# Performance work log

Measured on AMD Instinct MI355X. Metric: run time of the kernel, lower is better.

The kernel has to match this reference:

```python
import jax, jax.numpy as jnp
import numpy as np

N_BINS = 15


def setup_inputs() -> dict:
    key = jax.random.key(0)
    k1, k2 = jax.random.split(key)
    probs = jax.random.uniform(k1, (1, 2, 4096, 4096), dtype=jnp.float32)
    labels = jax.random.randint(k2, (1, 1, 4096, 4096), 0, 2, dtype=jnp.int32)
    return {"probs": probs, "labels": labels}


def _bin_stats(conf, acc, boundaries):
    # bin i holds conf in (boundaries[i], boundaries[i+1]] -> searchsorted left - 1
    idx = jnp.searchsorted(boundaries, conf, side="left") - 1
    valid = (idx >= 0) & (idx < N_BINS)
    idx = jnp.where(valid, idx, N_BINS)  # route invalid (conf==0) to overflow bin
    vmask = valid.astype(conf.dtype)
    count = jax.ops.segment_sum(vmask, idx, num_segments=N_BINS + 1)[:N_BINS]
    csum = jax.ops.segment_sum(conf * vmask, idx, num_segments=N_BINS + 1)[:N_BINS]
    asum = jax.ops.segment_sum(acc * vmask, idx, num_segments=N_BINS + 1)[:N_BINS]
    return count, csum, asum


def reference(probs, labels):
    h, w = probs.shape[2], probs.shape[3]
    boundaries = jnp.linspace(0.0, 1.0, N_BINS + 1)
    conf0 = probs[0, 0].reshape(h * w)
    conf1 = probs[0, 1].reshape(h * w)
    lab = labels[0, 0].reshape(h * w)
    acc0 = (lab == 0).astype(probs.dtype)
    acc1 = (lab == 1).astype(probs.dtype)
    count0, csum0, asum0 = _bin_stats(conf0, acc0, boundaries)
    count1, csum1, asum1 = _bin_stats(conf1, acc1, boundaries)
    return (count0, csum0, asum0, count1, csum1, asum1)
```

## Files before the change

### kernel.cpp

```cpp
#include <hip/hip_runtime.h>
#include <stdint.h>


#define NBINS 15

__global__ void zero_out_kernel(float* out, int n) {
    int i = blockIdx.x * blockDim.x + threadIdx.x;
    if (i < n) out[i] = 0.0f;
}

__device__ __forceinline__ unsigned pack_u32(float c, int match, int* bin_out) {
    bool valid = (c > 0.0f) && (c <= 1.0f);
    float cb = fmaxf(fminf(c * 15.0f, 14.0f), 0.0f);
    *bin_out = (int)cb;
    unsigned cf = __float2uint_rn(fmaxf(c, 0.0f) * 2048.0f);
    unsigned v = (cf << 14) | ((match ? 1u : 0u) << 7) | 1u;
    return valid ? v : 0u;
}

__global__ __launch_bounds__(256, 4) void calib_hist_kernel(
        const float* __restrict__ probs, const int* __restrict__ labels,
        float* __restrict__ out, int npix) {
    __shared__ unsigned histA[16 * 256];
    __shared__ unsigned histB[16 * 256];
    int tid = threadIdx.x;
    #pragma unroll
    for (int k = 0; k < 16; ++k) {
        histA[k * 256 + tid] = 0u;
        histB[k * 256 + tid] = 0u;
    }
    __syncthreads();

    const float4* p0 = (const float4*)probs;
    const float4* p1 = (const float4*)(probs + npix);
    const int4*   lb = (const int4*)labels;
    int nvec   = npix >> 2;
    int stride = gridDim.x * blockDim.x;

    int i = blockIdx.x * blockDim.x + tid;
    if (i < nvec) {
        float4 a = p0[i], b = p1[i];
        int4   l = lb[i];
        while (true) {
            int  ni   = i + stride;
            bool more = ni < nvec;
            float4 a2, b2; int4 l2;
            if (more) { a2 = p0[ni]; b2 = p1[ni]; l2 = lb[ni]; }
            int bin; unsigned v;
            v = pack_u32(a.x, l.x == 0, &bin); histA[bin * 256 + tid] += v;
            v = pack_u32(b.x, l.x == 1, &bin); histB[bin * 256 + tid] += v;
            v = pack_u32(a.y, l.y == 0, &bin); histA[bin * 256 + tid] += v;
            v = pack_u32(b.y, l.y == 1, &bin); histB[bin * 256 + tid] += v;
            v = pack_u32(a.z, l.z == 0, &bin); histA[bin * 256 + tid] += v;
            v = pack_u32(b.z, l.z == 1, &bin); histB[bin * 256 + tid] += v;
            v = pack_u32(a.w, l.w == 0, &bin); histA[bin * 256 + tid] += v;
            v = pack_u32(b.w, l.w == 1, &bin); histB[bin * 256 + tid] += v;
            if (!more) break;
            i = ni; a = a2; b = b2; l = l2;
        }
    }
    __syncthreads();

    {
        int h   = tid;
        int e   = h >> 3, ch = e >> 4, bin = e & 15;
        const unsigned* src = ch ? histB : histA;
        unsigned cnt = 0, asum = 0, csum = 0;
        int base = (h & 7) * 32;
        #pragma unroll
        for (int j = 0; j < 32; ++j) {
            int col = base + ((j + h) & 31);
            unsigned x = src[bin * 256 + col];
            cnt  += x & 0x7Fu;
            asum += (x >> 7) & 0x7Fu;
            csum += x >> 14;
        }
        cnt  += __shfl_xor(cnt, 1); asum += __shfl_xor(asum, 1); csum += __shfl_xor(csum, 1);
        cnt  += __shfl_xor(cnt, 2); asum += __shfl_xor(asum, 2); csum += __shfl_xor(csum, 2);
        cnt  += __shfl_xor(cnt, 4); asum += __shfl_xor(asum, 4); csum += __shfl_xor(csum, 4);
        if ((h & 7) == 0 && bin < NBINS) {
            float* obase = out + ch * 45;
            atomicAdd(obase + bin,               (float)cnt);
            atomicAdd(obase + NBINS + bin,       (float)csum * (1.0f / 2048.0f));
            atomicAdd(obase + 2 * NBINS + bin,   (float)asum);
        }
    }
}

extern "C" void kernel_launch(void* const* d_in, const int* in_sizes, int n_in,
                              void* d_out, int out_size, void* d_ws, size_t ws_size,
                              hipStream_t stream) {
    const float* probs  = (const float*)d_in[0];
    const int*   labels = (const int*)d_in[1];
    float*       out    = (float*)d_out;
    int npix = in_sizes[1];

    zero_out_kernel<<<(out_size + 127) / 128, 128, 0, stream>>>(out, out_size);

    int nvec = npix >> 2;
    int blocks = (nvec + 256 * 16 - 1) / (256 * 16);
    if (blocks < 1) blocks = 1;
    calib_hist_kernel<<<blocks, 256, 0, stream>>>(probs, labels, out, npix);
}
```

Measured before the change: 292.6 us.

## Replace shared-memory per-thread histograms with register-resident predicated accumulators

```diff
diff --git a/kernel.cpp b/kernel.cpp
--- a/kernel.cpp
+++ b/kernel.cpp
@@ -18,59 +18,59 @@
     return valid ? v : 0u;
 }
 
+#define UPDATE16(acc, c, m)                                      \
+    do {                                                         \
+        int _bin; unsigned _v = pack_u32((c), (m), &_bin);       \
+        _Pragma("unroll")                                        \
+        for (int _k = 0; _k < 16; ++_k)                          \
+            (acc)[_k] += (_bin == _k) ? _v : 0u;                 \
+    } while (0)
+
 __global__ __launch_bounds__(256, 4) void calib_hist_kernel(
         const float* __restrict__ probs, const int* __restrict__ labels,
         float* __restrict__ out, int npix) {
-    __shared__ unsigned histA[16 * 256];
-    __shared__ unsigned histB[16 * 256];
-    int tid = threadIdx.x;
+    unsigned accA[16], accB[16];
     #pragma unroll
-    for (int k = 0; k < 16; ++k) {
-        histA[k * 256 + tid] = 0u;
-        histB[k * 256 + tid] = 0u;
-    }
-    __syncthreads();
+    for (int k = 0; k < 16; ++k) { accA[k] = 0u; accB[k] = 0u; }
 
     const float4* p0 = (const float4*)probs;
     const float4* p1 = (const float4*)(probs + npix);
     const int4*   lb = (const int4*)labels;
     int nvec   = npix >> 2;
     int stride = gridDim.x * blockDim.x;
+    int tid    = threadIdx.x;
 
-    int i = blockIdx.x * blockDim.x + tid;
-    if (i < nvec) {
-        float4 a = p0[i], b = p1[i];
+    for (int i = blockIdx.x * blockDim.x + tid; i < nvec; i += stride) {
+        float4 a = p0[i];
+        float4 b = p1[i];
         int4   l = lb[i];
-        while (true) {
-            int  ni   = i + stride;
-            bool more = ni < nvec;
-            float4 a2, b2; int4 l2;
-            if (more) { a2 = p0[ni]; b2 = p1[ni]; l2 = lb[ni]; }
-            int bin; unsigned v;
-            v = pack_u32(a.x, l.x == 0, &bin); histA[bin * 256 + tid] += v;
-            v = pack_u32(b.x, l.x == 1, &bin); histB[bin * 256 + tid] += v;
-            v = pack_u32(a.y, l.y == 0, &bin); histA[bin * 256 + tid] += v;
-            v = pack_u32(b.y, l.y == 1, &bin); histB[bin * 256 + tid] += v;
-            v = pack_u32(a.z, l.z == 0, &bin); histA[bin * 256 + tid] += v;
-            v = pack_u32(b.z, l.z == 1, &bin); histB[bin * 256 + tid] += v;
-            v = pack_u32(a.w, l.w == 0, &bin); histA[bin * 256 + tid] += v;
-            v = pack_u32(b.w, l.w == 1, &bin); histB[bin * 256 + tid] += v;
-            if (!more) break;
-            i = ni; a = a2; b = b2; l = l2;
-        }
+        UPDATE16(accA, a.x, l.x == 0);
+        UPDATE16(accB, b.x, l.x == 1);
+        UPDATE16(accA, a.y, l.y == 0);
+        UPDATE16(accB, b.y, l.y == 1);
+        UPDATE16(accA, a.z, l.z == 0);
+        UPDATE16(accB, b.z, l.z == 1);
+        UPDATE16(accA, a.w, l.w == 0);
+        UPDATE16(accB, b.w, l.w == 1);
+    }
+
+    __shared__ unsigned hist[32 * 256];
+    #pragma unroll
+    for (int k = 0; k < 16; ++k) {
+        hist[k * 256 + tid]        = accA[k];
+        hist[(16 + k) * 256 + tid] = accB[k];
     }
     __syncthreads();
 
     {
-        int h   = tid;
-        int e   = h >> 3, ch = e >> 4, bin = e & 15;
-        const unsigned* src = ch ? histB : histA;
+        int h = tid;
+        int e = h >> 3;
         unsigned cnt = 0, asum = 0, csum = 0;
         int base = (h & 7) * 32;
         #pragma unroll
         for (int j = 0; j < 32; ++j) {
             int col = base + ((j + h) & 31);
-            unsigned x = src[bin * 256 + col];
+            unsigned x = hist[e * 256 + col];
             cnt  += x & 0x7Fu;
             asum += (x >> 7) & 0x7Fu;
             csum += x >> 14;
@@ -78,11 +78,12 @@
         cnt  += __shfl_xor(cnt, 1); asum += __shfl_xor(asum, 1); csum += __shfl_xor(csum, 1);
         cnt  += __shfl_xor(cnt, 2); asum += __shfl_xor(asum, 2); csum += __shfl_xor(csum, 2);
         cnt  += __shfl_xor(cnt, 4); asum += __shfl_xor(asum, 4); csum += __shfl_xor(csum, 4);
+        int ch = e >> 4, bin = e & 15;
         if ((h & 7) == 0 && bin < NBINS) {
             float* obase = out + ch * 45;
-            atomicAdd(obase + bin,               (float)cnt);
-            atomicAdd(obase + NBINS + bin,       (float)csum * (1.0f / 2048.0f));
-            atomicAdd(obase + 2 * NBINS + bin,   (float)asum);
+            atomicAdd(obase + bin,             (float)cnt);
+            atomicAdd(obase + NBINS + bin,     (float)csum * (1.0f / 2048.0f));
+            atomicAdd(obase + 2 * NBINS + bin, (float)asum);
         }
     }
 }
@@ -97,8 +98,5 @@
 
     zero_out_kernel<<<(out_size + 127) / 128, 128, 0, stream>>>(out, out_size);
 
-    int nvec = npix >> 2;
-    int blocks = (nvec + 256 * 16 - 1) / (256 * 16);
-    if (blocks < 1) blocks = 1;
-    calib_hist_kernel<<<blocks, 256, 0, stream>>>(probs, labels, out, npix);
+    calib_hist_kernel<<<1280, 256, 0, stream>>>(probs, labels, out, npix);
 }
```

Result: slower. 316.4 us (+8.1%).
